# Kernel optimization log

Hardware: AMD Instinct MI355X
Metric: run time of the kernel (lower is better)

The kernel has to match this reference:

```python
import jax, jax.numpy as jnp
import numpy as np


def _build_cost_volume(l, r, D):
    """Vectorized equivalent of the 64-iteration shifted slice-write loop.

    cost[:, :C, i, :, w] = l[:, :, :, w]       for w >= i, else 0
    cost[:, C:, i, :, w] = r[:, :, :, w - i]   for w >= i, else 0
    Returns [B, 2C, D, H, W].
    """
    B, C, H, W = l.shape
    d = jnp.arange(D)[:, None]          # [D, 1]
    w = jnp.arange(W)[None, :]          # [1, W]
    mask = (w >= d)[None, None, :, None, :]   # [1, 1, D, 1, W]
    left = jnp.where(mask, l[:, :, None, :, :], 0.0)            # [B, C, D, H, W]
    idx = jnp.clip(w - d, 0, W - 1)                              # [D, W]
    right = r[:, :, :, idx]                                      # [B, C, H, D, W]
    right = jnp.transpose(right, (0, 1, 3, 2, 4))                # [B, C, D, H, W]
    right = jnp.where(mask, right, 0.0)
    return jnp.concatenate([left, right], axis=1)                # [B, 2C, D, H, W]


def setup_inputs() -> dict:
    key = jax.random.key(0)
    k0, k1, k2, k3 = jax.random.split(key, 4)
    shape = (1, 32, 96, 240)  # [B, C_feat, H/3, W/3]
    return {
        "l0": jax.random.normal(k0, shape, dtype=jnp.float32),
        "r0": jax.random.normal(k1, shape, dtype=jnp.float32),
        "l1": jax.random.normal(k2, shape, dtype=jnp.float32),
        "r1": jax.random.normal(k3, shape, dtype=jnp.float32),
        "max_disp": 192,
    }


def reference(l0, r0, l1, r1, max_disp):
    D = max_disp // 3  # 64 disparity levels at 1/3 resolution
    cost0 = _build_cost_volume(l0, r0, D)
    cost1 = _build_cost_volume(l1, r1, D)
    return jnp.stack([cost0, cost1])  # [2, B, 2C, D, H, W]
```

## Files before the change

### kernel.cpp

```cpp
#include <hip/hip_runtime.h>

#define CC   32
#define HH   96
#define WW   240
#define DD   64
#define W4   60
#define HQ   4
#define NHQ  (HH / HQ)
#define SLICE_F4 (HH * W4)

typedef float vf4 __attribute__((ext_vector_type(4)));

__global__ __launch_bounds__(256) void cost_volume_kernel(
        const float* __restrict__ l0, const float* __restrict__ r0,
        const float* __restrict__ l1, const float* __restrict__ r1,
        float* __restrict__ out) {
    unsigned b = blockIdx.x;
    const unsigned hq   = b % NHQ;  b /= NHQ;
    const unsigned c    = b & (CC - 1u);  b >>= 5;
    const unsigned half = b & 1u;
    const unsigned s    = b >> 1;

    const unsigned tid = threadIdx.x;
    if (tid >= 240) return;
    const unsigned r   = tid / 60u;
    const unsigned col = tid - r * 60u;
    const int w0 = (int)(col * 4u);

    const float* img = half ? (s ? r1 : r0) : (s ? l1 : l0);
    const vf4* row4 = reinterpret_cast<const vf4*>(img + (c * HH + hq * HQ + r) * WW);

    size_t of = (size_t)((s * 2u + half) * CC + c) * DD * SLICE_F4
              + (size_t)(hq * HQ + r) * W4 + col;
    vf4* o4 = reinterpret_cast<vf4*>(out);

    if (!half) {
        const vf4 x = row4[col];
#pragma unroll 4
        for (int d = 0; d < DD; ++d) {
            const int a = w0 - d;
            vf4 v;
            v.x = (a + 0 >= 0) ? x.x : 0.0f;
            v.y = (a + 1 >= 0) ? x.y : 0.0f;
            v.z = (a + 2 >= 0) ? x.z : 0.0f;
            v.w = (a + 3 >= 0) ? x.w : 0.0f;
            o4[of] = v;
            of += SLICE_F4;
        }
    } else {
#pragma unroll 2
        for (int q = 0; q < 16; ++q) {
            int iB = (int)col - q; if (iB < 0) iB = 0;
            int iA = iB - 1;       if (iA < 0) iA = 0;
            const vf4 B = row4[iB];
            const vf4 A = row4[iA];
            const int a0 = w0 - 4 * q;

            {
                vf4 v = B;
                v.x = (a0 + 0 >= 0) ? v.x : 0.0f;
                v.y = (a0 + 1 >= 0) ? v.y : 0.0f;
                v.z = (a0 + 2 >= 0) ? v.z : 0.0f;
                v.w = (a0 + 3 >= 0) ? v.w : 0.0f;
                o4[of] = v;  of += SLICE_F4;
            }
            {
                vf4 v = __builtin_shufflevector(A, B, 3, 4, 5, 6);
                const int a = a0 - 1;
                v.x = (a + 0 >= 0) ? v.x : 0.0f;
                v.y = (a + 1 >= 0) ? v.y : 0.0f;
                v.z = (a + 2 >= 0) ? v.z : 0.0f;
                v.w = (a + 3 >= 0) ? v.w : 0.0f;
                o4[of] = v;  of += SLICE_F4;
            }
            {
                vf4 v = __builtin_shufflevector(A, B, 2, 3, 4, 5);
                const int a = a0 - 2;
                v.x = (a + 0 >= 0) ? v.x : 0.0f;
                v.y = (a + 1 >= 0) ? v.y : 0.0f;
                v.z = (a + 2 >= 0) ? v.z : 0.0f;
                v.w = (a + 3 >= 0) ? v.w : 0.0f;
                o4[of] = v;  of += SLICE_F4;
            }
            {
                vf4 v = __builtin_shufflevector(A, B, 1, 2, 3, 4);
                const int a = a0 - 3;
                v.x = (a + 0 >= 0) ? v.x : 0.0f;
                v.y = (a + 1 >= 0) ? v.y : 0.0f;
                v.z = (a + 2 >= 0) ? v.z : 0.0f;
                v.w = (a + 3 >= 0) ? v.w : 0.0f;
                o4[of] = v;  of += SLICE_F4;
            }
        }
    }
}

extern "C" void kernel_launch(void* const* d_in, const int* in_sizes, int n_in,
                              void* d_out, int out_size, void* d_ws, size_t ws_size,
                              hipStream_t stream) {
    const float* l0 = (const float*)d_in[0];
    const float* r0 = (const float*)d_in[1];
    const float* l1 = (const float*)d_in[2];
    const float* r1 = (const float*)d_in[3];
    float* out = (float*)d_out;

    const unsigned nBlocks = 2u * 2u * CC * NHQ;
    hipLaunchKernelGGL(cost_volume_kernel, dim3(nBlocks), dim3(256), 0, stream,
                       l0, r0, l1, r1, out);
}
```

Baseline: 148.3 us.

## Restructure cost-volume blocks with LDS-staged right image and nontemporal stores

Reorganizes the grid so each 320-thread block covers half the rows of one channel for 32 disparities, with each thread handling nine float4 columns. Right-image rows are staged in shared memory and shifted from there, and all output writes use nontemporal stores to avoid polluting caches on this write-dominated kernel. This uses far fewer blocks and about 46 KB of LDS per right block, which may limit occupancy.

```diff
diff --git a/kernel.cpp b/kernel.cpp
--- a/kernel.cpp
+++ b/kernel.cpp
@@ -5,91 +5,127 @@
 #define WW   240
 #define DD   64
 #define W4   60
-#define HQ   4
-#define NHQ  (HH / HQ)
-#define SLICE_F4 (HH * W4)
+#define SLICE_F4  (HH * W4)
+#define HALF_ROWS 48
+#define HALF_F4   (HALF_ROWS * W4)
+#define THREADS   320
+#define NF4       9
 
 typedef float vf4 __attribute__((ext_vector_type(4)));
 
-__global__ __launch_bounds__(256) void cost_volume_kernel(
+__global__ __launch_bounds__(THREADS) void cost_volume_kernel(
         const float* __restrict__ l0, const float* __restrict__ r0,
         const float* __restrict__ l1, const float* __restrict__ r1,
         float* __restrict__ out) {
-    unsigned b = blockIdx.x;
-    const unsigned hq   = b % NHQ;  b /= NHQ;
-    const unsigned c    = b & (CC - 1u);  b >>= 5;
-    const unsigned half = b & 1u;
-    const unsigned s    = b >> 1;
+    const unsigned b    = blockIdx.x;
+    const unsigned hh   = b & 1u;
+    const unsigned dh   = (b >> 1) & 1u;
+    const unsigned g    = b >> 2;
+    const unsigned s    = g & 1u;
+    const unsigned cout = g >> 1;
+    const int d0 = (int)(dh * 32u);
+
+    const bool left  = (cout < CC);
+    const unsigned c = left ? cout : (cout - CC);
+    const float* img = left ? (s ? l1 : l0) : (s ? r1 : r0);
+    const vf4* win4  = reinterpret_cast<const vf4*>(img + (c * HH + hh * HALF_ROWS) * WW);
 
     const unsigned tid = threadIdx.x;
-    if (tid >= 240) return;
-    const unsigned r   = tid / 60u;
-    const unsigned col = tid - r * 60u;
-    const int w0 = (int)(col * 4u);
 
-    const float* img = half ? (s ? r1 : r0) : (s ? l1 : l0);
-    const vf4* row4 = reinterpret_cast<const vf4*>(img + (c * HH + hq * HQ + r) * WW);
+    vf4* o4 = reinterpret_cast<vf4*>(out)
+            + (size_t)((s * 64u + cout) * DD + (unsigned)d0) * SLICE_F4
+            + hh * HALF_F4;
 
-    size_t of = (size_t)((s * 2u + half) * CC + c) * DD * SLICE_F4
-              + (size_t)(hq * HQ + r) * W4 + col;
-    vf4* o4 = reinterpret_cast<vf4*>(out);
+    unsigned jj[NF4], colv[NF4];
+#pragma unroll
+    for (int k = 0; k < NF4; ++k) {
+        jj[k]   = tid + (unsigned)k * THREADS;
+        colv[k] = jj[k] % 60u;
+    }
 
-    if (!half) {
-        const vf4 x = row4[col];
+    if (left) {
+        vf4 x[NF4];
+#pragma unroll
+        for (int k = 0; k < NF4; ++k) x[k] = win4[jj[k]];
+
 #pragma unroll 4
-        for (int d = 0; d < DD; ++d) {
-            const int a = w0 - d;
-            vf4 v;
-            v.x = (a + 0 >= 0) ? x.x : 0.0f;
-            v.y = (a + 1 >= 0) ? x.y : 0.0f;
-            v.z = (a + 2 >= 0) ? x.z : 0.0f;
-            v.w = (a + 3 >= 0) ? x.w : 0.0f;
-            o4[of] = v;
-            of += SLICE_F4;
-        }
-    } else {
-#pragma unroll 2
-        for (int q = 0; q < 16; ++q) {
-            int iB = (int)col - q; if (iB < 0) iB = 0;
-            int iA = iB - 1;       if (iA < 0) iA = 0;
-            const vf4 B = row4[iB];
-            const vf4 A = row4[iA];
-            const int a0 = w0 - 4 * q;
-
-            {
-                vf4 v = B;
-                v.x = (a0 + 0 >= 0) ? v.x : 0.0f;
-                v.y = (a0 + 1 >= 0) ? v.y : 0.0f;
-                v.z = (a0 + 2 >= 0) ? v.z : 0.0f;
-                v.w = (a0 + 3 >= 0) ? v.w : 0.0f;
-                o4[of] = v;  of += SLICE_F4;
-            }
-            {
-                vf4 v = __builtin_shufflevector(A, B, 3, 4, 5, 6);
-                const int a = a0 - 1;
+        for (int t = 0; t < 32; ++t) {
+            const int dd = d0 + t;
+            vf4* op = o4 + (size_t)t * SLICE_F4;
+#pragma unroll
+            for (int k = 0; k < NF4; ++k) {
+                const int a = (int)(colv[k] * 4u) - dd;
+                vf4 v = x[k];
                 v.x = (a + 0 >= 0) ? v.x : 0.0f;
                 v.y = (a + 1 >= 0) ? v.y : 0.0f;
                 v.z = (a + 2 >= 0) ? v.z : 0.0f;
                 v.w = (a + 3 >= 0) ? v.w : 0.0f;
-                o4[of] = v;  of += SLICE_F4;
+                __builtin_nontemporal_store(v, &op[jj[k]]);
             }
-            {
-                vf4 v = __builtin_shufflevector(A, B, 2, 3, 4, 5);
-                const int a = a0 - 2;
+        }
+    } else {
+        __shared__ vf4 lds4[HALF_F4];
+#pragma unroll
+        for (int k = 0; k < NF4; ++k) lds4[jj[k]] = win4[jj[k]];
+        __syncthreads();
+
+        const int qbase = d0 >> 2;
+        for (int qg = 0; qg < 8; ++qg) {
+            const int q = qbase + qg;
+            vf4 A[NF4], B[NF4];
+#pragma unroll
+            for (int k = 0; k < NF4; ++k) {
+                int cb = (int)colv[k] - q; if (cb < 0) cb = 0;
+                int ca = cb - 1;           if (ca < 0) ca = 0;
+                const unsigned rowbase = jj[k] - colv[k];
+                B[k] = lds4[rowbase + (unsigned)cb];
+                A[k] = lds4[rowbase + (unsigned)ca];
+            }
+            const int dd0 = d0 + qg * 4;
+            vf4* op = o4 + (size_t)(qg * 4) * SLICE_F4;
+
+#pragma unroll
+            for (int k = 0; k < NF4; ++k) {
+                const int a = (int)(colv[k] * 4u) - dd0;
+                vf4 v = B[k];
                 v.x = (a + 0 >= 0) ? v.x : 0.0f;
                 v.y = (a + 1 >= 0) ? v.y : 0.0f;
                 v.z = (a + 2 >= 0) ? v.z : 0.0f;
                 v.w = (a + 3 >= 0) ? v.w : 0.0f;
-                o4[of] = v;  of += SLICE_F4;
+                __builtin_nontemporal_store(v, &op[jj[k]]);
             }
-            {
-                vf4 v = __builtin_shufflevector(A, B, 1, 2, 3, 4);
-                const int a = a0 - 3;
+            op += SLICE_F4;
+#pragma unroll
+            for (int k = 0; k < NF4; ++k) {
+                const int a = (int)(colv[k] * 4u) - dd0 - 1;
+                vf4 v = __builtin_shufflevector(A[k], B[k], 3, 4, 5, 6);
                 v.x = (a + 0 >= 0) ? v.x : 0.0f;
                 v.y = (a + 1 >= 0) ? v.y : 0.0f;
                 v.z = (a + 2 >= 0) ? v.z : 0.0f;
                 v.w = (a + 3 >= 0) ? v.w : 0.0f;
-                o4[of] = v;  of += SLICE_F4;
+                __builtin_nontemporal_store(v, &op[jj[k]]);
+            }
+            op += SLICE_F4;
+#pragma unroll
+            for (int k = 0; k < NF4; ++k) {
+                const int a = (int)(colv[k] * 4u) - dd0 - 2;
+                vf4 v = __builtin_shufflevector(A[k], B[k], 2, 3, 4, 5);
+                v.x = (a + 0 >= 0) ? v.x : 0.0f;
+                v.y = (a + 1 >= 0) ? v.y : 0.0f;
+                v.z = (a + 2 >= 0) ? v.z : 0.0f;
+                v.w = (a + 3 >= 0) ? v.w : 0.0f;
+                __builtin_nontemporal_store(v, &op[jj[k]]);
+            }
+            op += SLICE_F4;
+#pragma unroll
+            for (int k = 0; k < NF4; ++k) {
+                const int a = (int)(colv[k] * 4u) - dd0 - 3;
+                vf4 v = __builtin_shufflevector(A[k], B[k], 1, 2, 3, 4);
+                v.x = (a + 0 >= 0) ? v.x : 0.0f;
+                v.y = (a + 1 >= 0) ? v.y : 0.0f;
+                v.z = (a + 2 >= 0) ? v.z : 0.0f;
+                v.w = (a + 3 >= 0) ? v.w : 0.0f;
+                __builtin_nontemporal_store(v, &op[jj[k]]);
             }
         }
     }
@@ -104,7 +140,6 @@
     const float* r1 = (const float*)d_in[3];
     float* out = (float*)d_out;
 
-    const unsigned nBlocks = 2u * 2u * CC * NHQ;
-    hipLaunchKernelGGL(cost_volume_kernel, dim3(nBlocks), dim3(256), 0, stream,
+    hipLaunchKernelGGL(cost_volume_kernel, dim3(512), dim3(THREADS), 0, stream,
                        l0, r0, l1, r1, out);
 }
```

New measurement: 150.4 us. About the same (+1.4%).
